# Kernel optimization log

Hardware: AMD Instinct MI355X
Metric: run time of the kernel (lower is better)

## Reference

```python
import jax, jax.numpy as jnp
import numpy as np

B, S, C = 64, 1024, 512   # batch, flattened feature positions, cnn.n_features
V = 140                   # vocab size
A = 512                   # attn_size
H = 512                   # hidden_size
T = 128                   # max_length (labels.shape[1])


def _lin(k, out_dim, in_dim):
    w = jax.random.normal(k, (out_dim, in_dim), jnp.float32) / np.sqrt(in_dim)
    return w


def setup_inputs() -> dict:
    key = jax.random.key(0)
    ks = jax.random.split(key, 12)
    return {
        "image_features": jax.random.normal(ks[0], (B, S, C), jnp.float32),
        "labels": jax.random.randint(ks[1], (B, T), 0, V),
        # Ic: n_features -> attn_size
        "Ic_w": _lin(ks[2], A, C), "Ic_b": jnp.zeros((A,), jnp.float32),
        # Hc: hidden -> attn_size
        "Hc_w": _lin(ks[3], A, H), "Hc_b": jnp.zeros((A,), jnp.float32),
        # LSTMCell: input_size = V + A, gates stacked [i,f,g,o] like torch
        "W_ih": _lin(ks[4], 4 * H, V + A), "b_ih": jnp.zeros((4 * H,), jnp.float32),
        "W_hh": _lin(ks[5], 4 * H, H), "b_hh": jnp.zeros((4 * H,), jnp.float32),
        # character_distribution: hidden -> vocab
        "Wout": _lin(ks[6], V, H), "b_out": jnp.zeros((V,), jnp.float32),
    }


def reference(image_features, labels, Ic_w, Ic_b, Hc_w, Hc_b,
              W_ih, b_ih, W_hh, b_hh, Wout, b_out):
    # embed_image -> Ic projection once (keys == values in the attention)
    keys = jnp.einsum('bsc,ac->bsa', image_features, Ic_w) + Ic_b  # [B,S,A]
    inv_sqrt_a = 1.0 / np.sqrt(A)

    rnn_input0 = jax.nn.one_hot(labels[:, 0], V, dtype=jnp.float32)  # <sos> one-hot
    h0 = jnp.zeros((B, H), jnp.float32)
    c0 = jnp.zeros((B, H), jnp.float32)

    def step(carry, _):
        h, c, x_in = carry
        # per-timestep attention: query = Hc(hidden)
        q = h @ Hc_w.T + Hc_b                                  # [B,A]
        scores = jnp.einsum('ba,bsa->bs', q, keys) * inv_sqrt_a  # [B,S]
        w = jax.nn.softmax(scores, axis=-1)
        ctx = jnp.einsum('bs,bsa->ba', w, keys)                 # [B,A]
        # LSTMCell on cat(one_hot_input, context)
        x = jnp.concatenate([x_in, ctx], axis=-1)               # [B,V+A]
        gates = x @ W_ih.T + b_ih + h @ W_hh.T + b_hh           # [B,4H]
        i, f, g, o = jnp.split(gates, 4, axis=-1)
        c_new = jax.nn.sigmoid(f) * c + jax.nn.sigmoid(i) * jnp.tanh(g)
        h_new = jax.nn.sigmoid(o) * jnp.tanh(c_new)
        out = h_new @ Wout.T + b_out                            # [B,V] logits
        # inference path (no teacher forcing): re-embed argmax as one-hot
        nxt = jax.nn.one_hot(jnp.argmax(out, axis=-1), V, dtype=jnp.float32)
        return (h_new, c_new, nxt), out

    _, outs = jax.lax.scan(step, (h0, c0, rnn_input0), None, length=T)
    return jnp.transpose(outs, (1, 0, 2))  # [B,T,V]
```

## Files before the change

### kernel.cpp

```cpp
#include <hip/hip_runtime.h>
#include <math.h>

#define BB 64
#define SS 1024
#define CC 512
#define VV 140
#define AA 512
#define HH 512
#define TT 128
#define G4 2048
#define VA 652


__global__ void k_small(const float* __restrict__ Hc, const float* __restrict__ Hcb,
                        const float* __restrict__ Ic, const float* __restrict__ Icb,
                        float* __restrict__ p0, float* __restrict__ v0,
                        float* __restrict__ s0) {
    int t = threadIdx.x;
    float av = 0.f, pv = 0.f;
    for (int a = 0; a < AA; a++) {
        av += Hc[a * HH + t] * Icb[a];
        pv += Hcb[a] * Ic[a * CC + t];
    }
    v0[t] = av;
    p0[t] = pv;
    if (t == 0) {
        float s = 0.f;
        for (int a = 0; a < AA; a++) s += Hcb[a] * Icb[a];
        s0[0] = s;
    }
}

__global__ __launch_bounds__(256) void k_P(const float* __restrict__ Hc,
                                           const float* __restrict__ Ic,
                                           float* __restrict__ P) {
    int k = blockIdx.y;
    int c = blockIdx.x * 256 + threadIdx.x;
    float acc = 0.f;
    for (int a = 0; a < AA; a++) acc += Hc[a * HH + k] * Ic[a * CC + c];
    P[k * CC + c] = acc;
}

__global__ __launch_bounds__(256) void k_G(const float* __restrict__ Wih,
                                           const float* __restrict__ Ic,
                                           float* __restrict__ Gtmp) {
    int gb = blockIdx.y * 8;
    int c = blockIdx.x * 256 + threadIdx.x;
    float acc[8];
#pragma unroll
    for (int j = 0; j < 8; j++) acc[j] = 0.f;
    for (int a = 0; a < AA; a++) {
        float ic = Ic[a * CC + c];
#pragma unroll
        for (int j = 0; j < 8; j++) acc[j] += Wih[(size_t)(gb + j) * VA + VV + a] * ic;
    }
#pragma unroll
    for (int j = 0; j < 8; j++) Gtmp[(size_t)(gb + j) * CC + c] = acc[j];
}

__global__ void k_gate_bias(const float* __restrict__ Wih, const float* __restrict__ Icb,
                            const float* __restrict__ bih, const float* __restrict__ bhh,
                            float* __restrict__ gate_bias) {
    int g = blockIdx.x * 256 + threadIdx.x;
    float acc = bih[g] + bhh[g];
    for (int a = 0; a < AA; a++) acc += Wih[(size_t)g * VA + VV + a] * Icb[a];
    gate_bias[g] = acc;
}

__global__ void k_transpose(const float* __restrict__ src, float* __restrict__ dst,
                            int R, int Cc, int ld, int col0) {
    __shared__ float tile[32][33];
    int r0 = blockIdx.y * 32, c0 = blockIdx.x * 32;
    int tx = threadIdx.x, ty = threadIdx.y;
#pragma unroll
    for (int k = 0; k < 4; k++) {
        int r = r0 + ty + k * 8, c = c0 + tx;
        if (r < R && c < Cc) tile[ty + k * 8][tx] = src[(size_t)r * ld + col0 + c];
    }
    __syncthreads();
#pragma unroll
    for (int k = 0; k < 4; k++) {
        int c = c0 + ty + k * 8, r = r0 + tx;
        if (c < Cc && r < R) dst[(size_t)c * R + r] = tile[tx][ty + k * 8];
    }
}

__global__ void k_init(const int* __restrict__ labels, const float* __restrict__ p0,
                       const float* __restrict__ s0, float* __restrict__ h,
                       float* __restrict__ cst, float* __restrict__ qp,
                       float* __restrict__ qb, int* __restrict__ charr) {
    int b = blockIdx.x, t = threadIdx.x;
    h[b * HH + t] = 0.f;
    cst[b * HH + t] = 0.f;
    qp[b * CC + t] = p0[t];
    if (t == 0) {
        qb[b] = s0[0];
        charr[b] = labels[b * TT];
    }
}


#define ONLINE_UPDATE(score, xv)                                      \
    if ((score) > m) {                                                \
        float f_ = expf(m - (score));                                 \
        l = l * f_ + 1.f;                                             \
        _Pragma("unroll")                                             \
        for (int j = 0; j < 8; j++) acc[j] = acc[j] * f_ + (xv)[j];   \
        m = (score);                                                  \
    } else {                                                          \
        float p_ = expf((score) - m);                                 \
        l += p_;                                                      \
        _Pragma("unroll")                                             \
        for (int j = 0; j < 8; j++) acc[j] += p_ * (xv)[j];           \
    }

#define DOT8(xv) ((xv)[0] * qa.x + (xv)[1] * qa.y + (xv)[2] * qa.z + (xv)[3] * qa.w + \
                  (xv)[4] * qb4.x + (xv)[5] * qb4.y + (xv)[6] * qb4.z + (xv)[7] * qb4.w)

#define UNPACK8(xv, ra, rb) \
    (xv)[0] = ra.x; (xv)[1] = ra.y; (xv)[2] = ra.z; (xv)[3] = ra.w; \
    (xv)[4] = rb.x; (xv)[5] = rb.y; (xv)[6] = rb.z; (xv)[7] = rb.w;

__global__ __launch_bounds__(512) void k_flash(const float* __restrict__ X,
                                               const float* __restrict__ qp,
                                               const float* __restrict__ qb,
                                               float* __restrict__ part_m,
                                               float* __restrict__ part_l,
                                               float* __restrict__ part_acc) {
    int b = blockIdx.y, chunk = blockIdx.x;
    int tid = threadIdx.x, w = tid >> 6, lane = tid & 63;
    const float inv_sqrt_a = 0.044194173824159216f;

    const float4* q4 = (const float4*)(qp + b * CC) + lane * 2;
    float4 qa = q4[0], qb4 = q4[1];
    float qoff = qb[b];

    float m = -INFINITY, l = 0.f;
    float acc[8];
#pragma unroll
    for (int j = 0; j < 8; j++) acc[j] = 0.f;

    int s0 = chunk * 256 + w * 32;
    const float* base = X + ((size_t)b * SS + s0) * CC;
    for (int i = 0; i < 32; i += 4) {
        const float4* xr0 = (const float4*)(base + (size_t)(i + 0) * CC) + lane * 2;
        const float4* xr1 = (const float4*)(base + (size_t)(i + 1) * CC) + lane * 2;
        const float4* xr2 = (const float4*)(base + (size_t)(i + 2) * CC) + lane * 2;
        const float4* xr3 = (const float4*)(base + (size_t)(i + 3) * CC) + lane * 2;
        float4 x0a = xr0[0], x0b = xr0[1];
        float4 x1a = xr1[0], x1b = xr1[1];
        float4 x2a = xr2[0], x2b = xr2[1];
        float4 x3a = xr3[0], x3b = xr3[1];
        float xv0[8], xv1[8], xv2[8], xv3[8];
        UNPACK8(xv0, x0a, x0b);
        UNPACK8(xv1, x1a, x1b);
        UNPACK8(xv2, x2a, x2b);
        UNPACK8(xv3, x3a, x3b);
        float d0 = DOT8(xv0);
        float d1 = DOT8(xv1);
        float d2 = DOT8(xv2);
        float d3 = DOT8(xv3);
#pragma unroll
        for (int off = 1; off < 64; off <<= 1) {
            d0 += __shfl_xor(d0, off, 64);
            d1 += __shfl_xor(d1, off, 64);
            d2 += __shfl_xor(d2, off, 64);
            d3 += __shfl_xor(d3, off, 64);
        }
        float sc0 = (d0 + qoff) * inv_sqrt_a;
        float sc1 = (d1 + qoff) * inv_sqrt_a;
        float sc2 = (d2 + qoff) * inv_sqrt_a;
        float sc3 = (d3 + qoff) * inv_sqrt_a;
        ONLINE_UPDATE(sc0, xv0);
        ONLINE_UPDATE(sc1, xv1);
        ONLINE_UPDATE(sc2, xv2);
        ONLINE_UPDATE(sc3, xv3);
    }

    __shared__ float lm[8], ll[8];
    __shared__ __align__(16) float lacc[8][512];
    if (lane == 0) lm[w] = m;
    __syncthreads();
    float M = lm[0];
#pragma unroll
    for (int j = 1; j < 8; j++) M = fmaxf(M, lm[j]);
    float f = expf(m - M);
    if (lane == 0) ll[w] = l * f;
#pragma unroll
    for (int j = 0; j < 8; j++) lacc[w][lane * 8 + j] = acc[j] * f;
    __syncthreads();
    float s = 0.f;
#pragma unroll
    for (int j = 0; j < 8; j++) s += lacc[j][tid];
    part_acc[((b * 4 + chunk) << 9) + tid] = s;
    if (tid == 0) {
        float lt = 0.f;
        for (int j = 0; j < 8; j++) lt += ll[j];
        part_m[b * 4 + chunk] = M;
        part_l[b * 4 + chunk] = lt;
    }
}

__global__ __launch_bounds__(256) void k_gates(const float* __restrict__ part_m,
                                               const float* __restrict__ part_l,
                                               const float* __restrict__ part_acc,
                                               const float* __restrict__ h,
                                               const float* __restrict__ GT,
                                               const float* __restrict__ WhhT,
                                               float* __restrict__ pg) {
    int cs = blockIdx.x, gt = blockIdx.y, bt = blockIdx.z;
    int tid = threadIdx.x;
    int tg = tid & 63, tb = tid >> 6;

    __shared__ __align__(16) float actT[128 * 16];
    __shared__ float coefL[16][4];
    __shared__ __align__(16) float wbuf[32 * 256];

    if (cs < 4) {
        if (tid < 16) {
            int b = bt * 16 + tid;
            float m0 = part_m[b * 4 + 0], m1 = part_m[b * 4 + 1];
            float m2 = part_m[b * 4 + 2], m3 = part_m[b * 4 + 3];
            float M = fmaxf(fmaxf(m0, m1), fmaxf(m2, m3));
            float e0 = expf(m0 - M), e1 = expf(m1 - M), e2 = expf(m2 - M), e3 = expf(m3 - M);
            float denom = e0 * part_l[b * 4 + 0] + e1 * part_l[b * 4 + 1] +
                          e2 * part_l[b * 4 + 2] + e3 * part_l[b * 4 + 3];
            float inv = 1.f / denom;
            coefL[tid][0] = e0 * inv; coefL[tid][1] = e1 * inv;
            coefL[tid][2] = e2 * inv; coefL[tid][3] = e3 * inv;
        }
        __syncthreads();
#pragma unroll
        for (int k = 0; k < 8; k++) {
            int idx = k * 256 + tid;
            int bb = idx >> 7, cc = idx & 127;
            int b = bt * 16 + bb;
            const float* pa = part_acc + (size_t)(b * 4) * 512 + cs * 128 + cc;
            float v = coefL[bb][0] * pa[0] + coefL[bb][1] * pa[512] +
                      coefL[bb][2] * pa[1024] + coefL[bb][3] * pa[1536];
            actT[cc * 16 + bb] = v;
        }
    } else {
#pragma unroll
        for (int k = 0; k < 8; k++) {
            int idx = k * 256 + tid;
            int bb = idx >> 7, cc = idx & 127;
            actT[cc * 16 + bb] = h[(bt * 16 + bb) * HH + (cs - 4) * 128 + cc];
        }
    }

    const float* W = (cs < 4) ? (GT + (size_t)(cs * 128) * G4)
                              : (WhhT + (size_t)((cs - 4) * 128) * G4);
    float4 acc0 = make_float4(0, 0, 0, 0), acc1 = make_float4(0, 0, 0, 0);
    float4 acc2 = make_float4(0, 0, 0, 0), acc3 = make_float4(0, 0, 0, 0);

#define FMA4(accv, sclr, wv)                    \
    accv.x += (sclr) * wv.x; accv.y += (sclr) * wv.y; \
    accv.z += (sclr) * wv.z; accv.w += (sclr) * wv.w;

    for (int cchunk = 0; cchunk < 4; cchunk++) {
        __syncthreads();
#pragma unroll
        for (int k = 0; k < 32; k++) {
            int idx = k * 256 + tid;
            int i = idx >> 8, j = idx & 255;
            wbuf[idx] = W[(size_t)(cchunk * 32 + i) * G4 + gt * 256 + j];
        }
        __syncthreads();
#pragma unroll 4
        for (int i = 0; i < 32; i++) {
            float4 wv = *(const float4*)&wbuf[i * 256 + tg * 4];
            float4 av = *(const float4*)&actT[(cchunk * 32 + i) * 16 + tb * 4];
            FMA4(acc0, av.x, wv);
            FMA4(acc1, av.y, wv);
            FMA4(acc2, av.z, wv);
            FMA4(acc3, av.w, wv);
        }
    }
#undef FMA4

    int b0 = bt * 16 + tb * 4;
    int g0 = gt * 256 + tg * 4;
    *(float4*)&pg[(size_t)(cs * BB + b0 + 0) * G4 + g0] = acc0;
    *(float4*)&pg[(size_t)(cs * BB + b0 + 1) * G4 + g0] = acc1;
    *(float4*)&pg[(size_t)(cs * BB + b0 + 2) * G4 + g0] = acc2;
    *(float4*)&pg[(size_t)(cs * BB + b0 + 3) * G4 + g0] = acc3;
}

__global__ __launch_bounds__(512) void k_update(
    const float* __restrict__ pg, const float* __restrict__ gate_bias,
    const float* __restrict__ Wih0T, const float* __restrict__ Wout,
    const float* __restrict__ bout, const float* __restrict__ v0,
    const float* __restrict__ s0, float* __restrict__ h, float* __restrict__ cst,
    float* __restrict__ qb, int* __restrict__ charr, float* __restrict__ out, int t) {
    int b = blockIdx.x, tid = threadIdx.x;
    __shared__ __align__(16) float gl[G4];
    __shared__ __align__(16) float hl[HH];
    __shared__ float logl[VV];

    int ch = charr[b];

    {
        int g0 = tid * 4;
        float4 a = *(const float4*)&gate_bias[g0];
        float4 wv = *(const float4*)&Wih0T[(size_t)ch * G4 + g0];
        a.x += wv.x; a.y += wv.y; a.z += wv.z; a.w += wv.w;
#pragma unroll
        for (int j = 0; j < 8; j++) {
            float4 p = *(const float4*)&pg[(size_t)(j * BB + b) * G4 + g0];
            a.x += p.x; a.y += p.y; a.z += p.z; a.w += p.w;
        }
        *(float4*)&gl[g0] = a;
    }
    __syncthreads();

    {
        int idx = tid;
        float ig = 1.f / (1.f + expf(-gl[idx]));
        float fg = 1.f / (1.f + expf(-gl[512 + idx]));
        float gg = tanhf(gl[1024 + idx]);
        float og = 1.f / (1.f + expf(-gl[1536 + idx]));
        float cn = fg * cst[b * HH + idx] + ig * gg;
        float hn = og * tanhf(cn);
        cst[b * HH + idx] = cn;
        h[b * HH + idx] = hn;
        hl[idx] = hn;
    }
    __syncthreads();

    int w = tid >> 6, lane = tid & 63;
    const float4* hr = (const float4*)hl + lane * 2;
    float4 h0 = hr[0], h1 = hr[1];
    for (int v = w; v < VV; v += 8) {
        const float4* wr = (const float4*)(Wout + (size_t)v * HH) + lane * 2;
        float4 w0 = wr[0], w1 = wr[1];
        float d = w0.x * h0.x + w0.y * h0.y + w0.z * h0.z + w0.w * h0.w +
                  w1.x * h1.x + w1.y * h1.y + w1.z * h1.z + w1.w * h1.w;
#pragma unroll
        for (int off = 1; off < 64; off <<= 1) d += __shfl_xor(d, off, 64);
        if (lane == 0) {
            d += bout[v];
            logl[v] = d;
            out[((size_t)b * TT + t) * VV + v] = d;
        }
    }
    __syncthreads();

    if (w == 0) {
        float bv = logl[lane];
        int bi = lane;
        for (int v = lane + 64; v < VV; v += 64) {
            float x = logl[v];
            if (x > bv) { bv = x; bi = v; }
        }
#pragma unroll
        for (int off = 1; off < 64; off <<= 1) {
            float ov = __shfl_xor(bv, off, 64);
            int oi = __shfl_xor(bi, off, 64);
            if (ov > bv || (ov == bv && oi < bi)) { bv = ov; bi = oi; }
        }
        if (lane == 0) charr[b] = bi;
    } else if (w == 1) {
        float p = 0.f;
#pragma unroll
        for (int j = 0; j < 8; j++) {
            int k = lane + 64 * j;
            p += hl[k] * v0[k];
        }
#pragma unroll
        for (int off = 1; off < 64; off <<= 1) p += __shfl_xor(p, off, 64);
        if (lane == 0) qb[b] = p + s0[0];
    }
}

__global__ __launch_bounds__(256) void k_qp(const float* __restrict__ h,
                                            const float* __restrict__ P,
                                            const float* __restrict__ p0,
                                            float* __restrict__ qp) {
    int ct = blockIdx.x;
    int bg = blockIdx.y;
    int tid = threadIdx.x;
    int cl = tid & 63, kq = tid >> 6;
    int b0 = bg * 2;

    __shared__ __align__(16) float hlT[HH][2];
    __shared__ float red[4][2][64];

    for (int i = tid; i < 2 * HH; i += 256) {
        int j = i >> 9, k = i & (HH - 1);
        hlT[k][j] = h[(size_t)(b0 + j) * HH + k];
    }
    __syncthreads();

    int c = ct * 64 + cl;
    const float* Pp = P + (size_t)(kq * 128) * CC + c;
    float a0 = 0.f, a1 = 0.f;
#pragma unroll 8
    for (int kk = 0; kk < 128; kk++) {
        float pv = Pp[(size_t)kk * CC];
        float2 hv = *(const float2*)&hlT[kq * 128 + kk][0];
        a0 += hv.x * pv;
        a1 += hv.y * pv;
    }
    red[kq][0][cl] = a0;
    red[kq][1][cl] = a1;
    __syncthreads();

    if (kq == 0) {
        float base = p0[c];
        float r0 = red[0][0][cl] + red[1][0][cl] + red[2][0][cl] + red[3][0][cl] + base;
        float r1 = red[0][1][cl] + red[1][1][cl] + red[2][1][cl] + red[3][1][cl] + base;
        qp[(size_t)(b0 + 0) * CC + c] = r0;
        qp[(size_t)(b0 + 1) * CC + c] = r1;
    }
}


extern "C" void kernel_launch(void* const* d_in, const int* in_sizes, int n_in,
                              void* d_out, int out_size, void* d_ws, size_t ws_size,
                              hipStream_t stream) {
    const float* X    = (const float*)d_in[0];
    const int*   lab  = (const int*)d_in[1];
    const float* Icw  = (const float*)d_in[2];
    const float* Icb  = (const float*)d_in[3];
    const float* Hcw  = (const float*)d_in[4];
    const float* Hcb  = (const float*)d_in[5];
    const float* Wih  = (const float*)d_in[6];
    const float* bih  = (const float*)d_in[7];
    const float* Whh  = (const float*)d_in[8];
    const float* bhh  = (const float*)d_in[9];
    const float* Wout = (const float*)d_in[10];
    const float* bout = (const float*)d_in[11];
    float* out = (float*)d_out;

    float* ws = (float*)d_ws;
    size_t off = 0;
    float* P        = ws + off; off += 512 * 512;
    float* GT       = ws + off; off += 512 * 2048;
    float* WhhT     = ws + off; off += 512 * 2048;
    float* Wih0T    = ws + off; off += 140 * 2048;
    float* gateb    = ws + off; off += 2048;
    float* p0       = ws + off; off += 512;
    float* v0       = ws + off; off += 512;
    float* s0       = ws + off; off += 64;
    float* h        = ws + off; off += 64 * 512;
    float* cst      = ws + off; off += 64 * 512;
    float* qp       = ws + off; off += 64 * 512;
    float* qb       = ws + off; off += 64;
    float* part_m   = ws + off; off += 256;
    float* part_l   = ws + off; off += 256;
    float* part_acc = ws + off; off += 64 * 4 * 512;
    float* pg       = ws + off; off += 8 * 64 * 2048;
    int*   charr    = (int*)(ws + off); off += 64;
    if (ws_size < off * sizeof(float)) return;

    float* Gtmp = pg;

    k_small<<<1, 512, 0, stream>>>(Hcw, Hcb, Icw, Icb, p0, v0, s0);
    k_P<<<dim3(2, 512), 256, 0, stream>>>(Hcw, Icw, P);
    k_G<<<dim3(2, 256), 256, 0, stream>>>(Wih, Icw, Gtmp);
    k_transpose<<<dim3(16, 64), dim3(32, 8), 0, stream>>>(Gtmp, GT, 2048, 512, 512, 0);
    k_transpose<<<dim3(16, 64), dim3(32, 8), 0, stream>>>(Whh, WhhT, 2048, 512, 512, 0);
    k_transpose<<<dim3(5, 64), dim3(32, 8), 0, stream>>>(Wih, Wih0T, 2048, 140, 652, 0);
    k_gate_bias<<<8, 256, 0, stream>>>(Wih, Icb, bih, bhh, gateb);
    k_init<<<64, 512, 0, stream>>>(lab, p0, s0, h, cst, qp, qb, charr);

    for (int t = 0; t < TT; t++) {
        k_flash<<<dim3(4, 64), 512, 0, stream>>>(X, qp, qb, part_m, part_l, part_acc);
        k_gates<<<dim3(8, 8, 4), 256, 0, stream>>>(part_m, part_l, part_acc, h, GT, WhhT, pg);
        k_update<<<64, 512, 0, stream>>>(pg, gateb, Wih0T, Wout, bout, v0, s0,
                                         h, cst, qb, charr, out, t);
        k_qp<<<dim3(8, 32), 256, 0, stream>>>(h, P, p0, qp);
    }
}
```

Before: 8.126 ms.

## Fuse LSTM update and query projection into one kernel with double-buffered state

Merges the per-step LSTM cell/logits/argmax kernel and the query-projection kernel into a single kernel launched with 4 blocks per batch row. Every block recomputes the LSTM cell state locally in shared memory, so each can project its own 128-column slice of qp without a separate launch. Only the first block of each row writes h, the cell state, the logits and the next character. Cell state and character arrays are double-buffered so blocks of the same row never read values another block has already overwritten. This removes one kernel launch and its dependency gap per timestep, at the cost of redundantly reading the gate partials and recomputing the cell four times per row.

```diff
diff --git a/kernel.cpp b/kernel.cpp
--- a/kernel.cpp
+++ b/kernel.cpp
@@ -87,15 +87,15 @@
 
 __global__ void k_init(const int* __restrict__ labels, const float* __restrict__ p0,
                        const float* __restrict__ s0, float* __restrict__ h,
-                       float* __restrict__ cst, float* __restrict__ qp,
-                       float* __restrict__ qb, int* __restrict__ charr) {
+                       float* __restrict__ cstA, float* __restrict__ qp,
+                       float* __restrict__ qb, int* __restrict__ charrA) {
     int b = blockIdx.x, t = threadIdx.x;
     h[b * HH + t] = 0.f;
-    cst[b * HH + t] = 0.f;
+    cstA[b * HH + t] = 0.f;
     qp[b * CC + t] = p0[t];
     if (t == 0) {
         qb[b] = s0[0];
-        charr[b] = labels[b * TT];
+        charrA[b] = labels[b * TT];
     }
 }
 
@@ -287,18 +287,26 @@
     *(float4*)&pg[(size_t)(cs * BB + b0 + 3) * G4 + g0] = acc3;
 }
 
-__global__ __launch_bounds__(512) void k_update(
+__global__ __launch_bounds__(512) void k_updqp(
     const float* __restrict__ pg, const float* __restrict__ gate_bias,
     const float* __restrict__ Wih0T, const float* __restrict__ Wout,
     const float* __restrict__ bout, const float* __restrict__ v0,
-    const float* __restrict__ s0, float* __restrict__ h, float* __restrict__ cst,
-    float* __restrict__ qb, int* __restrict__ charr, float* __restrict__ out, int t) {
-    int b = blockIdx.x, tid = threadIdx.x;
+    const float* __restrict__ s0, const float* __restrict__ P,
+    const float* __restrict__ p0,
+    const float* __restrict__ cin, float* __restrict__ cout,
+    const int* __restrict__ chin, int* __restrict__ chout,
+    float* __restrict__ h, float* __restrict__ qp, float* __restrict__ qb,
+    float* __restrict__ out, int t) {
+    int bx = blockIdx.x, tid = threadIdx.x;
+    int cb = bx >> 2, quad = bx & 3;
+    int w = tid >> 6, lane = tid & 63;
+
     __shared__ __align__(16) float gl[G4];
     __shared__ __align__(16) float hl[HH];
     __shared__ float logl[VV];
-
-    int ch = charr[b];
+    __shared__ float red[512];
+
+    int ch = chin[cb];
 
     {
         int g0 = tid * 4;
@@ -307,7 +315,7 @@
         a.x += wv.x; a.y += wv.y; a.z += wv.z; a.w += wv.w;
 #pragma unroll
         for (int j = 0; j < 8; j++) {
-            float4 p = *(const float4*)&pg[(size_t)(j * BB + b) * G4 + g0];
+            float4 p = *(const float4*)&pg[(size_t)(j * BB + cb) * G4 + g0];
             a.x += p.x; a.y += p.y; a.z += p.z; a.w += p.w;
         }
         *(float4*)&gl[g0] = a;
@@ -315,103 +323,80 @@
     __syncthreads();
 
     {
-        int idx = tid;
-        float ig = 1.f / (1.f + expf(-gl[idx]));
-        float fg = 1.f / (1.f + expf(-gl[512 + idx]));
-        float gg = tanhf(gl[1024 + idx]);
-        float og = 1.f / (1.f + expf(-gl[1536 + idx]));
-        float cn = fg * cst[b * HH + idx] + ig * gg;
+        float ig = 1.f / (1.f + expf(-gl[tid]));
+        float fg = 1.f / (1.f + expf(-gl[512 + tid]));
+        float gg = tanhf(gl[1024 + tid]);
+        float og = 1.f / (1.f + expf(-gl[1536 + tid]));
+        float cn = fg * cin[cb * HH + tid] + ig * gg;
         float hn = og * tanhf(cn);
-        cst[b * HH + idx] = cn;
-        h[b * HH + idx] = hn;
-        hl[idx] = hn;
-    }
-    __syncthreads();
-
-    int w = tid >> 6, lane = tid & 63;
-    const float4* hr = (const float4*)hl + lane * 2;
-    float4 h0 = hr[0], h1 = hr[1];
-    for (int v = w; v < VV; v += 8) {
-        const float4* wr = (const float4*)(Wout + (size_t)v * HH) + lane * 2;
-        float4 w0 = wr[0], w1 = wr[1];
-        float d = w0.x * h0.x + w0.y * h0.y + w0.z * h0.z + w0.w * h0.w +
-                  w1.x * h1.x + w1.y * h1.y + w1.z * h1.z + w1.w * h1.w;
-#pragma unroll
-        for (int off = 1; off < 64; off <<= 1) d += __shfl_xor(d, off, 64);
-        if (lane == 0) {
-            d += bout[v];
-            logl[v] = d;
-            out[((size_t)b * TT + t) * VV + v] = d;
-        }
-    }
-    __syncthreads();
-
-    if (w == 0) {
-        float bv = logl[lane];
-        int bi = lane;
-        for (int v = lane + 64; v < VV; v += 64) {
-            float x = logl[v];
-            if (x > bv) { bv = x; bi = v; }
-        }
-#pragma unroll
-        for (int off = 1; off < 64; off <<= 1) {
-            float ov = __shfl_xor(bv, off, 64);
-            int oi = __shfl_xor(bi, off, 64);
-            if (ov > bv || (ov == bv && oi < bi)) { bv = ov; bi = oi; }
-        }
-        if (lane == 0) charr[b] = bi;
-    } else if (w == 1) {
-        float p = 0.f;
-#pragma unroll
-        for (int j = 0; j < 8; j++) {
-            int k = lane + 64 * j;
-            p += hl[k] * v0[k];
-        }
-#pragma unroll
-        for (int off = 1; off < 64; off <<= 1) p += __shfl_xor(p, off, 64);
-        if (lane == 0) qb[b] = p + s0[0];
-    }
-}
-
-__global__ __launch_bounds__(256) void k_qp(const float* __restrict__ h,
-                                            const float* __restrict__ P,
-                                            const float* __restrict__ p0,
-                                            float* __restrict__ qp) {
-    int ct = blockIdx.x;
-    int bg = blockIdx.y;
-    int tid = threadIdx.x;
-    int cl = tid & 63, kq = tid >> 6;
-    int b0 = bg * 2;
-
-    __shared__ __align__(16) float hlT[HH][2];
-    __shared__ float red[4][2][64];
-
-    for (int i = tid; i < 2 * HH; i += 256) {
-        int j = i >> 9, k = i & (HH - 1);
-        hlT[k][j] = h[(size_t)(b0 + j) * HH + k];
-    }
-    __syncthreads();
-
-    int c = ct * 64 + cl;
-    const float* Pp = P + (size_t)(kq * 128) * CC + c;
-    float a0 = 0.f, a1 = 0.f;
+        if (quad == 0) {
+            cout[cb * HH + tid] = cn;
+            h[cb * HH + tid] = hn;
+        }
+        hl[tid] = hn;
+    }
+    __syncthreads();
+
+    if (quad == 0) {
+        const float4* hr = (const float4*)hl + lane * 2;
+        float4 h0 = hr[0], h1 = hr[1];
+        for (int v = w; v < VV; v += 8) {
+            const float4* wr = (const float4*)(Wout + (size_t)v * HH) + lane * 2;
+            float4 w0 = wr[0], w1 = wr[1];
+            float d = w0.x * h0.x + w0.y * h0.y + w0.z * h0.z + w0.w * h0.w +
+                      w1.x * h1.x + w1.y * h1.y + w1.z * h1.z + w1.w * h1.w;
+#pragma unroll
+            for (int off = 1; off < 64; off <<= 1) d += __shfl_xor(d, off, 64);
+            if (lane == 0) {
+                d += bout[v];
+                logl[v] = d;
+                out[((size_t)cb * TT + t) * VV + v] = d;
+            }
+        }
+        __syncthreads();
+
+        if (w == 0) {
+            float bv = logl[lane];
+            int bi = lane;
+            for (int v = lane + 64; v < VV; v += 64) {
+                float x = logl[v];
+                if (x > bv) { bv = x; bi = v; }
+            }
+#pragma unroll
+            for (int off = 1; off < 64; off <<= 1) {
+                float ov = __shfl_xor(bv, off, 64);
+                int oi = __shfl_xor(bi, off, 64);
+                if (ov > bv || (ov == bv && oi < bi)) { bv = ov; bi = oi; }
+            }
+            if (lane == 0) chout[cb] = bi;
+        } else if (w == 1) {
+            float p = 0.f;
+#pragma unroll
+            for (int j = 0; j < 8; j++) {
+                int k = lane + 64 * j;
+                p += hl[k] * v0[k];
+            }
+#pragma unroll
+            for (int off = 1; off < 64; off <<= 1) p += __shfl_xor(p, off, 64);
+            if (lane == 0) qb[cb] = p + s0[0];
+        }
+    }
+
+    {
+        int cl = tid & 127, kq = tid >> 7;
+        int c = quad * 128 + cl;
+        const float* Pp = P + (size_t)(kq * 128) * CC + c;
+        float a = 0.f;
 #pragma unroll 8
-    for (int kk = 0; kk < 128; kk++) {
-        float pv = Pp[(size_t)kk * CC];
-        float2 hv = *(const float2*)&hlT[kq * 128 + kk][0];
-        a0 += hv.x * pv;
-        a1 += hv.y * pv;
-    }
-    red[kq][0][cl] = a0;
-    red[kq][1][cl] = a1;
-    __syncthreads();
-
-    if (kq == 0) {
-        float base = p0[c];
-        float r0 = red[0][0][cl] + red[1][0][cl] + red[2][0][cl] + red[3][0][cl] + base;
-        float r1 = red[0][1][cl] + red[1][1][cl] + red[2][1][cl] + red[3][1][cl] + base;
-        qp[(size_t)(b0 + 0) * CC + c] = r0;
-        qp[(size_t)(b0 + 1) * CC + c] = r1;
+        for (int kk = 0; kk < 128; kk++)
+            a += hl[kq * 128 + kk] * Pp[(size_t)kk * CC];
+        red[kq * 128 + cl] = a;
+    }
+    __syncthreads();
+    if (tid < 128) {
+        int c = quad * 128 + tid;
+        float r = red[tid] + red[128 + tid] + red[256 + tid] + red[384 + tid] + p0[c];
+        qp[(size_t)cb * CC + c] = r;
     }
 }
 
@@ -444,14 +429,16 @@
     float* v0       = ws + off; off += 512;
     float* s0       = ws + off; off += 64;
     float* h        = ws + off; off += 64 * 512;
-    float* cst      = ws + off; off += 64 * 512;
+    float* cstA     = ws + off; off += 64 * 512;
+    float* cstB     = ws + off; off += 64 * 512;
     float* qp       = ws + off; off += 64 * 512;
     float* qb       = ws + off; off += 64;
     float* part_m   = ws + off; off += 256;
     float* part_l   = ws + off; off += 256;
     float* part_acc = ws + off; off += 64 * 4 * 512;
     float* pg       = ws + off; off += 8 * 64 * 2048;
-    int*   charr    = (int*)(ws + off); off += 64;
+    int*   charrA   = (int*)(ws + off); off += 64;
+    int*   charrB   = (int*)(ws + off); off += 64;
     if (ws_size < off * sizeof(float)) return;
 
     float* Gtmp = pg;
@@ -463,13 +450,16 @@
     k_transpose<<<dim3(16, 64), dim3(32, 8), 0, stream>>>(Whh, WhhT, 2048, 512, 512, 0);
     k_transpose<<<dim3(5, 64), dim3(32, 8), 0, stream>>>(Wih, Wih0T, 2048, 140, 652, 0);
     k_gate_bias<<<8, 256, 0, stream>>>(Wih, Icb, bih, bhh, gateb);
-    k_init<<<64, 512, 0, stream>>>(lab, p0, s0, h, cst, qp, qb, charr);
+    k_init<<<64, 512, 0, stream>>>(lab, p0, s0, h, cstA, qp, qb, charrA);
 
     for (int t = 0; t < TT; t++) {
+        const float* cin = (t & 1) ? cstB : cstA;
+        float* cout      = (t & 1) ? cstA : cstB;
+        const int* chin  = (t & 1) ? charrB : charrA;
+        int* chout       = (t & 1) ? charrA : charrB;
         k_flash<<<dim3(4, 64), 512, 0, stream>>>(X, qp, qb, part_m, part_l, part_acc);
         k_gates<<<dim3(8, 8, 4), 256, 0, stream>>>(part_m, part_l, part_acc, h, GT, WhhT, pg);
-        k_update<<<64, 512, 0, stream>>>(pg, gateb, Wih0T, Wout, bout, v0, s0,
-                                         h, cst, qb, charr, out, t);
-        k_qp<<<dim3(8, 32), 256, 0, stream>>>(h, P, p0, qp);
-    }
-}
+        k_updqp<<<256, 512, 0, stream>>>(pg, gateb, Wih0T, Wout, bout, v0, s0, P, p0,
+                                         cin, cout, chin, chout, h, qp, qb, out, t);
+    }
+}
```

Result: no change. 7.978 ms (-1.8%).
